# Performance work log

Hardware: AMD Instinct MI355X
Metric: run time of the kernel (lower is better)

## Reference

```python
import jax, jax.numpy as jnp
import numpy as np

B, C, H, W = 8, 64, 256, 256
NUM_HEADS = 4
ROPE_BASE = 10000.0


def dwconv(x, w, b, groups):
    # x: (B, Cin, H, W), w: (Cout, Cin//groups, 3, 3), padding=1 stride=1 -> SAME
    y = jax.lax.conv_general_dilated(
        x, w, window_strides=(1, 1), padding='SAME',
        feature_group_count=groups,
        dimension_numbers=('NCHW', 'OIHW', 'NCHW'))
    return y + b[None, :, None, None]


def rope(x4):
    # Faithful to torch RoPE: rotations shape (h, c//2) complex, broadcast
    # against (b, h, w, c//2) -> rotation angle indexed by the *w* axis.
    b, h, w, c = x4.shape
    k_max = c // 2
    theta = 1.0 / (ROPE_BASE ** (jnp.arange(k_max, dtype=x4.dtype) / k_max))
    angles = jnp.arange(h, dtype=x4.dtype)[:, None] * theta[None, :]  # (h, k_max)
    cos, sin = jnp.cos(angles), jnp.sin(angles)
    xr = x4.reshape(b, h, w, k_max, 2)
    xre, xim = xr[..., 0], xr[..., 1]
    re = xre * cos - xim * sin
    im = xre * sin + xim * cos
    return jnp.stack([re, im], axis=-1).reshape(b, h, w, c)


def setup_inputs() -> dict:
    key = jax.random.key(0)
    k1, k2, k3, k4, k5 = jax.random.split(key, 5)
    x = jax.random.normal(k1, (B, C, H, W), dtype=jnp.float32)
    # depthwise qk conv: groups=C, out=2C -> weight (2C, 1, 3, 3)
    qk_w = jax.random.normal(k2, (2 * C, 1, 3, 3), dtype=jnp.float32) * 0.1
    qk_b = jax.random.normal(k3, (2 * C,), dtype=jnp.float32) * 0.01
    # lepe depthwise conv: (C, 1, 3, 3)
    lepe_w = jax.random.normal(k4, (C, 1, 3, 3), dtype=jnp.float32) * 0.1
    lepe_b = jax.random.normal(k5, (C,), dtype=jnp.float32) * 0.01
    return {'x': x, 'qk_w': qk_w, 'qk_b': qk_b, 'lepe_w': lepe_w, 'lepe_b': lepe_b}


def reference(x, qk_w, qk_b, lepe_w, lepe_b):
    b = x.shape[0]
    c = x.shape[1]
    h, w = x.shape[2], x.shape[3]
    n = h * w
    num_heads = NUM_HEADS
    head_dim = c // num_heads

    qk = dwconv(x, qk_w, qk_b, groups=c)            # (b, 2c, h, w)
    # faithful raw reshapes (same row-major semantics as torch.reshape)
    qk = qk.reshape(b, n, 2 * c)
    xf = x.reshape(b, n, c)

    qk = qk.reshape(b, n, 2, c).transpose(2, 0, 1, 3)
    q, k, v = qk[0], qk[1], xf
    q = jax.nn.elu(q) + 1.0
    k = jax.nn.elu(k) + 1.0

    q_rope = rope(q.reshape(b, h, w, c)).reshape(b, n, num_heads, head_dim).transpose(0, 2, 1, 3)
    k_rope = rope(k.reshape(b, h, w, c)).reshape(b, n, num_heads, head_dim).transpose(0, 2, 1, 3)
    qh = q.reshape(b, n, num_heads, head_dim).transpose(0, 2, 1, 3)
    kh = k.reshape(b, n, num_heads, head_dim).transpose(0, 2, 1, 3)
    vh = v.reshape(b, n, num_heads, head_dim).transpose(0, 2, 1, 3)

    k_mean = kh.mean(axis=-2, keepdims=True)        # (b, heads, 1, hd)
    z = 1.0 / (jnp.einsum('bhnd,bhmd->bhnm', qh, k_mean) + 1e-6)  # (b, heads, n, 1)

    scale = n ** (-0.5)
    kv = jnp.einsum('bhnd,bhne->bhde', k_rope * scale, vh * scale)  # (b, heads, hd, hd)
    out = jnp.einsum('bhnd,bhde->bhne', q_rope, kv) * z             # (b, heads, n, hd)

    out = out.transpose(0, 2, 1, 3).reshape(b, n, c)
    v_img = vh.transpose(0, 2, 1, 3).reshape(b, h, w, c).transpose(0, 3, 1, 2)  # (b, c, h, w)
    lepe_out = dwconv(v_img, lepe_w, lepe_b, groups=c)
    out = out + lepe_out.transpose(0, 2, 3, 1).reshape(b, n, c)
    out = out.transpose(0, 2, 1).reshape(b, c, h, w)
    return out
```

## Files before the change

### kernel.cpp

```cpp
#include <hip/hip_runtime.h>
#include <math.h>

#define NB 8
#define NC 64
#define NHEADS 4
#define NTOK 65536

constexpr int CS_OFF = 0;
constexpr int KV_OFF = 16384;
constexpr int KM_OFF = 24576;

__global__ __launch_bounds__(256) void k0_setup(float* __restrict__ ws) {
    int i = blockIdx.x * 256 + threadIdx.x;
    if (i < 8192) {
        int w = i >> 5, p = i & 31;
        double th = pow(10000.0, -(double)p / 32.0);
        double ang = (double)w * th;
        ws[CS_OFF + 2 * i]     = (float)cos(ang);
        ws[CS_OFF + 2 * i + 1] = (float)sin(ang);
        ws[KV_OFF + i] = 0.0f;
        if (i < 512) ws[KM_OFF + i] = 0.0f;
    }
}

__global__ __launch_bounds__(256) void k1_kv(const float* __restrict__ x,
        const float* __restrict__ qkw, const float* __restrict__ qkb,
        float* __restrict__ ws) {
    const int b  = blockIdx.x >> 6;
    const int ch = blockIdx.x & 63;
    const int t  = threadIdx.x;
    const float* xb     = x + (size_t)b * (NC * NTOK);
    const float* xplane = xb + ch * NTOK;

    __shared__ float in_t[18][256];
    __shared__ float kr_t[64][64];
    __shared__ float v_t[64][64];
    __shared__ float wq[2][9];
    __shared__ float bq[2];
    __shared__ float red[256];

    if (t < 18) ((float*)wq)[t] = qkw[2 * ch * 9 + t];
    if (t < 2)  bq[t] = qkb[2 * ch + t];

    const int ck = t & 63;
    const int g  = t >> 6;
    const int d0 = ((t & 63) >> 3) << 1;
    const int e0 = (t & 7) << 1;
    const int h  = g;

    float km_acc = 0.f;
    float a00 = 0.f, a01 = 0.f, a10 = 0.f, a11 = 0.f;

    for (int y0 = 0; y0 < 256; y0 += 16) {
        for (int j = t; j < 18 * 64; j += 256) {
            int row = j >> 6, c4 = (j & 63) << 2;
            int y = y0 - 1 + row;
            float4 val = make_float4(0.f, 0.f, 0.f, 0.f);
            if (y >= 0 && y < 256)
                val = *(const float4*)(xplane + y * 256 + c4);
            *(float4*)(&in_t[row][c4]) = val;
        }
        for (int j = t; j < 64 * 16; j += 256) {
            int tok = j >> 4, f4 = (j & 15) << 2;
            int n = (2 * ch + (tok >> 5)) * 512 + 2 * y0 + (tok & 31);
            *(float4*)(&v_t[tok][f4]) = *(const float4*)(xb + (size_t)n * 64 + f4);
        }
        __syncthreads();

        #pragma unroll
        for (int co2 = 0; co2 < 2; ++co2)
        #pragma unroll
        for (int xb2 = 0; xb2 < 2; ++xb2)
        #pragma unroll
        for (int yi = 0; yi < 4; ++yi) {
            int yl = g + 4 * yi;
            int xx = xb2 * 128 + 64 + ck;
            float acc = bq[co2];
            #pragma unroll
            for (int ky = 0; ky < 3; ++ky)
            #pragma unroll
            for (int kx = 0; kx < 3; ++kx) {
                int xc = xx + kx - 1;
                float iv = (xc >= 0 && xc < 256) ? in_t[yl + ky][xc] : 0.f;
                acc = fmaf(wq[co2][ky * 3 + kx], iv, acc);
            }
            float kh = acc > 0.f ? acc + 1.f : expf(acc);
            km_acc += kh;
            int w_i = (2 * (y0 + yl) + xb2) & 255;
            float2 cs = *(const float2*)(ws + CS_OFF + (((w_i << 5) + (ck >> 1)) << 1));
            float partner = __shfl_xor(kh, 1);
            float kr = (ck & 1) ? fmaf(partner, cs.y, kh * cs.x)
                                : fmaf(-partner, cs.y, kh * cs.x);
            kr_t[co2 * 32 + yl * 2 + xb2][ck] = kr;
        }
        __syncthreads();

        #pragma unroll 8
        for (int tok = 0; tok < 64; ++tok) {
            float2 kk = *(const float2*)(&kr_t[tok][(h << 4) + d0]);
            float2 vv = *(const float2*)(&v_t[tok][(h << 4) + e0]);
            a00 = fmaf(kk.x, vv.x, a00);
            a01 = fmaf(kk.x, vv.y, a01);
            a10 = fmaf(kk.y, vv.x, a10);
            a11 = fmaf(kk.y, vv.y, a11);
        }
        __syncthreads();
    }

    float* kvg = ws + KV_OFF + ((b * 4 + h) * 16) * 16;
    atomicAdd(&kvg[(d0    ) * 16 + e0    ], a00);
    atomicAdd(&kvg[(d0    ) * 16 + e0 + 1], a01);
    atomicAdd(&kvg[(d0 + 1) * 16 + e0    ], a10);
    atomicAdd(&kvg[(d0 + 1) * 16 + e0 + 1], a11);

    red[t] = km_acc;
    __syncthreads();
    if (t < 64) {
        float s = red[t] + red[t + 64] + red[t + 128] + red[t + 192];
        atomicAdd(ws + KM_OFF + b * 64 + t, s);
    }
}

__global__ __launch_bounds__(256) void k3_out(const float* __restrict__ x,
        const float* __restrict__ qkw, const float* __restrict__ qkb,
        const float* __restrict__ lw, const float* __restrict__ lb,
        const float* __restrict__ ws, float* __restrict__ out) {
    const int b  = blockIdx.x >> 6;
    const int ch = blockIdx.x & 63;
    const int t  = threadIdx.x;
    const float* xb     = x + (size_t)b * (NC * NTOK);
    const float* xplane = xb + ch * NTOK;
    float* outb = out + (size_t)b * (NC * NTOK);

    __shared__ float in_t[18][256];
    __shared__ float q_t[64][65];
    __shared__ float o_t[64][65];
    __shared__ float wq[2][9];
    __shared__ float bq[2];
    __shared__ float lw_s[64][9];
    __shared__ float lb_s[64];

    if (t < 18) ((float*)wq)[t] = qkw[2 * ch * 9 + t];
    if (t < 2)  bq[t] = qkb[2 * ch + t];
    for (int j = t; j < 64 * 9; j += 256) ((float*)lw_s)[j] = lw[j];
    if (t < 64) lb_s[t] = lb[t];

    const int cq  = t & 63;
    const int g   = t >> 6;
    const int tok = t & 63;
    const int hu  = __builtin_amdgcn_readfirstlane(t >> 6);

    const float* kv_h = ws + KV_OFF + (b * 4 + hu) * 256;
    const float* km_h = ws + KM_OFF + b * 64 + hu * 16;
    const float inv_n = 1.0f / 65536.0f;

    for (int y0 = 0; y0 < 256; y0 += 16) {
        for (int j = t; j < 18 * 64; j += 256) {
            int row = j >> 6, c4 = (j & 63) << 2;
            int y = y0 - 1 + row;
            float4 val = make_float4(0.f, 0.f, 0.f, 0.f);
            if (y >= 0 && y < 256)
                val = *(const float4*)(xplane + y * 256 + c4);
            *(float4*)(&in_t[row][c4]) = val;
        }
        __syncthreads();

        #pragma unroll
        for (int co2 = 0; co2 < 2; ++co2)
        #pragma unroll
        for (int xb2 = 0; xb2 < 2; ++xb2)
        #pragma unroll
        for (int yi = 0; yi < 4; ++yi) {
            int yl = g + 4 * yi;
            int xx = xb2 * 128 + cq;
            float acc = bq[co2];
            #pragma unroll
            for (int ky = 0; ky < 3; ++ky)
            #pragma unroll
            for (int kx = 0; kx < 3; ++kx) {
                int xc = xx + kx - 1;
                float iv = (xc >= 0 && xc < 256) ? in_t[yl + ky][xc] : 0.f;
                acc = fmaf(wq[co2][ky * 3 + kx], iv, acc);
            }
            q_t[co2 * 32 + yl * 2 + xb2][cq] = acc > 0.f ? acc + 1.f : expf(acc);
        }
        __syncthreads();

        {
            int co2 = tok >> 5;
            int r   = 2 * y0 + (tok & 31);
            int w_i = r & 255;
            int Yim = (2 * ch + co2) * 2 + (r >> 8);

            float qv[16], qr[16];
            #pragma unroll
            for (int d = 0; d < 16; ++d) qv[d] = q_t[tok][hu * 16 + d];

            float zd = 0.f;
            #pragma unroll
            for (int d = 0; d < 16; ++d) zd = fmaf(qv[d], km_h[d], zd);
            float zinv = 1.0f / (zd * inv_n + 1e-6f);

            const float2* csp = (const float2*)(ws + CS_OFF) + (w_i << 5) + hu * 8;
            #pragma unroll
            for (int p = 0; p < 8; ++p) {
                float2 cs = csp[p];
                qr[2 * p]     = qv[2 * p] * cs.x - qv[2 * p + 1] * cs.y;
                qr[2 * p + 1] = qv[2 * p] * cs.y + qv[2 * p + 1] * cs.x;
            }

            float oa[16];
            #pragma unroll
            for (int e = 0; e < 16; ++e) oa[e] = 0.f;
            #pragma unroll
            for (int d = 0; d < 16; ++d) {
                float qd = qr[d];
                const float* kvr = kv_h + d * 16;
                #pragma unroll
                for (int e = 0; e < 16; ++e) oa[e] = fmaf(qd, kvr[e], oa[e]);
            }
            float zs = zinv * inv_n;

            float lp[16];
            #pragma unroll
            for (int e = 0; e < 16; ++e) lp[e] = lb_s[hu * 16 + e];
            #pragma unroll
            for (int dy = -1; dy <= 1; ++dy) {
                int Y2 = Yim + dy;
                if (Y2 < 0 || Y2 > 255) continue;
                #pragma unroll
                for (int dx = -1; dx <= 1; ++dx) {
                    int X2 = w_i + dx;
                    if (X2 < 0 || X2 > 255) continue;
                    const float* src = xb + ((size_t)(Y2 * 256 + X2)) * 64 + hu * 16;
                    float sv[16];
                    *(float4*)(&sv[0])  = *(const float4*)(src);
                    *(float4*)(&sv[4])  = *(const float4*)(src + 4);
                    *(float4*)(&sv[8])  = *(const float4*)(src + 8);
                    *(float4*)(&sv[12]) = *(const float4*)(src + 12);
                    int kt = (dy + 1) * 3 + (dx + 1);
                    #pragma unroll
                    for (int e = 0; e < 16; ++e)
                        lp[e] = fmaf(lw_s[hu * 16 + e][kt], sv[e], lp[e]);
                }
            }
            #pragma unroll
            for (int e = 0; e < 16; ++e)
                o_t[tok][hu * 16 + e] = fmaf(oa[e], zs, lp[e]);
        }
        __syncthreads();

        {
            int co2w = tok >> 5;
            size_t base = (size_t)((2 * ch + co2w) * 512 + 2 * y0 + (tok & 31));
            #pragma unroll
            for (int kk = 0; kk < 16; ++kk) {
                int c = g + 4 * kk;
                outb[(size_t)c * NTOK + base] = o_t[tok][c];
            }
        }
        __syncthreads();
    }
}

extern "C" void kernel_launch(void* const* d_in, const int* in_sizes, int n_in,
                              void* d_out, int out_size, void* d_ws, size_t ws_size,
                              hipStream_t stream) {
    const float* x   = (const float*)d_in[0];
    const float* qkw = (const float*)d_in[1];
    const float* qkb = (const float*)d_in[2];
    const float* lw  = (const float*)d_in[3];
    const float* lb  = (const float*)d_in[4];
    float* out = (float*)d_out;
    float* ws  = (float*)d_ws;

    hipLaunchKernelGGL(k0_setup, dim3(32),  dim3(256), 0, stream, ws);
    hipLaunchKernelGGL(k1_kv,    dim3(512), dim3(256), 0, stream, x, qkw, qkb, ws);
    hipLaunchKernelGGL(k3_out,   dim3(512), dim3(256), 0, stream, x, qkw, qkb, lw, lb, ws, out);
}
```

Before: 572.9 us.

## Split kv and output kernels across four row chunks and trim loaded columns

```diff
diff --git a/kernel.cpp b/kernel.cpp
--- a/kernel.cpp
+++ b/kernel.cpp
@@ -1,9 +1,7 @@
 #include <hip/hip_runtime.h>
 #include <math.h>
 
-#define NB 8
 #define NC 64
-#define NHEADS 4
 #define NTOK 65536
 
 constexpr int CS_OFF = 0;
@@ -26,18 +24,19 @@
 __global__ __launch_bounds__(256) void k1_kv(const float* __restrict__ x,
         const float* __restrict__ qkw, const float* __restrict__ qkb,
         float* __restrict__ ws) {
-    const int b  = blockIdx.x >> 6;
-    const int ch = blockIdx.x & 63;
+    const int idx = blockIdx.x;
+    const int b   = idx >> 8;
+    const int ch  = (idx & 255) >> 2;
+    const int ybase = (idx & 3) * 64;
     const int t  = threadIdx.x;
     const float* xb     = x + (size_t)b * (NC * NTOK);
     const float* xplane = xb + ch * NTOK;
 
-    __shared__ float in_t[18][256];
-    __shared__ float kr_t[64][64];
-    __shared__ float v_t[64][64];
+    __shared__ float in_t[10][140];
+    __shared__ float kr_t[32][64];
+    __shared__ float v_t[32][64];
     __shared__ float wq[2][9];
     __shared__ float bq[2];
-    __shared__ float red[256];
 
     if (t < 18) ((float*)wq)[t] = qkw[2 * ch * 9 + t];
     if (t < 2)  bq[t] = qkb[2 * ch + t];
@@ -51,18 +50,21 @@
     float km_acc = 0.f;
     float a00 = 0.f, a01 = 0.f, a10 = 0.f, a11 = 0.f;
 
-    for (int y0 = 0; y0 < 256; y0 += 16) {
-        for (int j = t; j < 18 * 64; j += 256) {
-            int row = j >> 6, c4 = (j & 63) << 2;
+    for (int y0 = ybase; y0 < ybase + 64; y0 += 8) {
+        for (int j = t; j < 10 * 35; j += 256) {
+            int row = j / 35, s = j - row * 35;
             int y = y0 - 1 + row;
+            int gcol, pos;
+            if (s < 18) { gcol = 60 + 4 * s;        pos = 4 * s; }
+            else        { gcol = 188 + 4 * (s - 18); pos = 72 + 4 * (s - 18); }
             float4 val = make_float4(0.f, 0.f, 0.f, 0.f);
             if (y >= 0 && y < 256)
-                val = *(const float4*)(xplane + y * 256 + c4);
-            *(float4*)(&in_t[row][c4]) = val;
-        }
-        for (int j = t; j < 64 * 16; j += 256) {
+                val = *(const float4*)(xplane + y * 256 + gcol);
+            *(float4*)(&in_t[row][pos]) = val;
+        }
+        for (int j = t; j < 32 * 16; j += 256) {
             int tok = j >> 4, f4 = (j & 15) << 2;
-            int n = (2 * ch + (tok >> 5)) * 512 + 2 * y0 + (tok & 31);
+            int n = (2 * ch + (tok >> 4)) * 512 + 2 * y0 + (tok & 15);
             *(float4*)(&v_t[tok][f4]) = *(const float4*)(xb + (size_t)n * 64 + f4);
         }
         __syncthreads();
@@ -72,16 +74,16 @@
         #pragma unroll
         for (int xb2 = 0; xb2 < 2; ++xb2)
         #pragma unroll
-        for (int yi = 0; yi < 4; ++yi) {
+        for (int yi = 0; yi < 2; ++yi) {
             int yl = g + 4 * yi;
-            int xx = xb2 * 128 + 64 + ck;
             float acc = bq[co2];
             #pragma unroll
             for (int ky = 0; ky < 3; ++ky)
             #pragma unroll
             for (int kx = 0; kx < 3; ++kx) {
-                int xc = xx + kx - 1;
-                float iv = (xc >= 0 && xc < 256) ? in_t[yl + ky][xc] : 0.f;
+                int xc = (xb2 ? 192 : 64) + ck + kx - 1;
+                int pos = xb2 ? xc - 116 : xc - 60;
+                float iv = (xb2 && xc >= 256) ? 0.f : in_t[yl + ky][pos];
                 acc = fmaf(wq[co2][ky * 3 + kx], iv, acc);
             }
             float kh = acc > 0.f ? acc + 1.f : expf(acc);
@@ -91,12 +93,12 @@
             float partner = __shfl_xor(kh, 1);
             float kr = (ck & 1) ? fmaf(partner, cs.y, kh * cs.x)
                                 : fmaf(-partner, cs.y, kh * cs.x);
-            kr_t[co2 * 32 + yl * 2 + xb2][ck] = kr;
+            kr_t[co2 * 16 + yl * 2 + xb2][ck] = kr;
         }
         __syncthreads();
 
         #pragma unroll 8
-        for (int tok = 0; tok < 64; ++tok) {
+        for (int tok = 0; tok < 32; ++tok) {
             float2 kk = *(const float2*)(&kr_t[tok][(h << 4) + d0]);
             float2 vv = *(const float2*)(&v_t[tok][(h << 4) + e0]);
             a00 = fmaf(kk.x, vv.x, a00);
@@ -113,6 +115,7 @@
     atomicAdd(&kvg[(d0 + 1) * 16 + e0    ], a10);
     atomicAdd(&kvg[(d0 + 1) * 16 + e0 + 1], a11);
 
+    float* red = &v_t[0][0];
     red[t] = km_acc;
     __syncthreads();
     if (t < 64) {
@@ -125,16 +128,20 @@
         const float* __restrict__ qkw, const float* __restrict__ qkb,
         const float* __restrict__ lw, const float* __restrict__ lb,
         const float* __restrict__ ws, float* __restrict__ out) {
-    const int b  = blockIdx.x >> 6;
-    const int ch = blockIdx.x & 63;
+    const int idx = blockIdx.x;
+    const int b   = idx >> 8;
+    const int ch  = (idx & 255) >> 2;
+    const int ybase = (idx & 3) * 64;
     const int t  = threadIdx.x;
     const float* xb     = x + (size_t)b * (NC * NTOK);
     const float* xplane = xb + ch * NTOK;
     float* outb = out + (size_t)b * (NC * NTOK);
 
-    __shared__ float in_t[18][256];
+    __shared__ union SU {
+        float in_t[18][140];
+        float o_t[64][65];
+    } u;
     __shared__ float q_t[64][65];
-    __shared__ float o_t[64][65];
     __shared__ float wq[2][9];
     __shared__ float bq[2];
     __shared__ float lw_s[64][9];
@@ -154,14 +161,17 @@
     const float* km_h = ws + KM_OFF + b * 64 + hu * 16;
     const float inv_n = 1.0f / 65536.0f;
 
-    for (int y0 = 0; y0 < 256; y0 += 16) {
-        for (int j = t; j < 18 * 64; j += 256) {
-            int row = j >> 6, c4 = (j & 63) << 2;
+    for (int y0 = ybase; y0 < ybase + 64; y0 += 16) {
+        for (int j = t; j < 18 * 35; j += 256) {
+            int row = j / 35, s = j - row * 35;
             int y = y0 - 1 + row;
+            int gcol, pos;
+            if (s < 17) { gcol = 4 * s;              pos = 4 * s; }
+            else        { gcol = 124 + 4 * (s - 17); pos = 68 + 4 * (s - 17); }
             float4 val = make_float4(0.f, 0.f, 0.f, 0.f);
             if (y >= 0 && y < 256)
-                val = *(const float4*)(xplane + y * 256 + c4);
-            *(float4*)(&in_t[row][c4]) = val;
+                val = *(const float4*)(xplane + y * 256 + gcol);
+            *(float4*)(&u.in_t[row][pos]) = val;
         }
         __syncthreads();
 
@@ -172,14 +182,14 @@
         #pragma unroll
         for (int yi = 0; yi < 4; ++yi) {
             int yl = g + 4 * yi;
-            int xx = xb2 * 128 + cq;
             float acc = bq[co2];
             #pragma unroll
             for (int ky = 0; ky < 3; ++ky)
             #pragma unroll
             for (int kx = 0; kx < 3; ++kx) {
-                int xc = xx + kx - 1;
-                float iv = (xc >= 0 && xc < 256) ? in_t[yl + ky][xc] : 0.f;
+                int xc = (xb2 ? 128 : 0) + cq + kx - 1;
+                int pos = xb2 ? xc - 56 : xc;
+                float iv = (!xb2 && xc < 0) ? 0.f : u.in_t[yl + ky][pos];
                 acc = fmaf(wq[co2][ky * 3 + kx], iv, acc);
             }
             q_t[co2 * 32 + yl * 2 + xb2][cq] = acc > 0.f ? acc + 1.f : expf(acc);
@@ -246,7 +256,7 @@
             }
             #pragma unroll
             for (int e = 0; e < 16; ++e)
-                o_t[tok][hu * 16 + e] = fmaf(oa[e], zs, lp[e]);
+                u.o_t[tok][hu * 16 + e] = fmaf(oa[e], zs, lp[e]);
         }
         __syncthreads();
 
@@ -256,7 +266,7 @@
             #pragma unroll
             for (int kk = 0; kk < 16; ++kk) {
                 int c = g + 4 * kk;
-                outb[(size_t)c * NTOK + base] = o_t[tok][c];
+                outb[(size_t)c * NTOK + base] = u.o_t[tok][c];
             }
         }
         __syncthreads();
@@ -274,7 +284,7 @@
     float* out = (float*)d_out;
     float* ws  = (float*)d_ws;
 
-    hipLaunchKernelGGL(k0_setup, dim3(32),  dim3(256), 0, stream, ws);
-    hipLaunchKernelGGL(k1_kv,    dim3(512), dim3(256), 0, stream, x, qkw, qkb, ws);
-    hipLaunchKernelGGL(k3_out,   dim3(512), dim3(256), 0, stream, x, qkw, qkb, lw, lb, ws, out);
-}
+    hipLaunchKernelGGL(k0_setup, dim3(32),   dim3(256), 0, stream, ws);
+    hipLaunchKernelGGL(k1_kv,    dim3(2048), dim3(256), 0, stream, x, qkw, qkb, ws);
+    hipLaunchKernelGGL(k3_out,   dim3(2048), dim3(256), 0, stream, x, qkw, qkb, lw, lb, ws, out);
+}
```

After: 535.8 us. 6.5% less time.
